# Kernel tuning notes

Hardware: AMD Instinct MI355X
Metric: run time of the kernel (lower is better)

The kernel has to match this reference:

```python
import jax, jax.numpy as jnp
import numpy as np

N, E, XD = 100000, 300000, 32
H, C = 4, 64          # heads, per-head out channels
D = H * C             # 256, node feature width
L = 3                 # num_message_passing
EPS = 1e-5
NEG_SLOPE = 0.2


def setup_inputs() -> dict:
    key = jax.random.key(0)
    ks = jax.random.split(key, 16)
    s = 0.05
    return {
        "x": jax.random.normal(ks[0], (N, XD), jnp.float32),
        "edge_index": jax.random.randint(ks[1], (2, E), 0, N, jnp.int32),
        "edge_type": jax.random.randint(ks[2], (E,), 0, 3, jnp.int32),
        "edge_feat": jax.random.uniform(ks[3], (E,), jnp.float32),
        # pre-encoder Linear(x_dim -> D)
        "W0": jax.random.normal(ks[4], (XD, D), jnp.float32) * s,
        "b0": jnp.zeros((D,), jnp.float32),
        # per-layer GATv2 params, stacked over L layers
        "Wl": jax.random.normal(ks[5], (L, D, D), jnp.float32) * s,
        "bl": jnp.zeros((L, D), jnp.float32),
        "Wr": jax.random.normal(ks[6], (L, D, D), jnp.float32) * s,
        "br": jnp.zeros((L, D), jnp.float32),
        "We": jax.random.normal(ks[7], (L, 4, D), jnp.float32) * s,  # lin_edge (no bias)
        "att": jax.random.normal(ks[8], (L, H, C), jnp.float32) * s,
        "bo": jnp.zeros((L, D), jnp.float32),
        # graph-mode LayerNorm (single module, reused every layer)
        "gamma": jnp.ones((D,), jnp.float32),
        "beta": jnp.zeros((D,), jnp.float32),
    }


def _graph_layernorm(h, gamma, beta):
    # PyG LayerNorm(mode='graph'): normalize over ALL nodes and features of the graph
    mu = jnp.mean(h)
    hc = h - mu
    var = jnp.mean(hc * hc)
    return hc * jax.lax.rsqrt(var + EPS) * gamma + beta


def _gatv2_layer(h, src, dst, eattr, Wl, bl, Wr, br, We, att, bo):
    xl = (h @ Wl + bl).reshape(N, H, C)
    xr = (h @ Wr + br).reshape(N, H, C)
    ea = (eattr @ We).reshape(E, H, C)
    e = jax.nn.leaky_relu(xl[src] + xr[dst] + ea, NEG_SLOPE)   # [E,H,C]
    alpha = jnp.einsum('ehc,hc->eh', e, att)                    # [E,H]
    amax = jax.ops.segment_max(alpha, dst, num_segments=N)     # [N,H]
    ex = jnp.exp(alpha - amax[dst])
    denom = jax.ops.segment_sum(ex, dst, num_segments=N)       # [N,H]
    a = ex / denom[dst]                                         # softmax per dst node
    msg = xl[src] * a[:, :, None]                               # [E,H,C]
    out = jax.ops.segment_sum(msg, dst, num_segments=N)        # [N,H,C]
    return out.reshape(N, D) + bo


def reference(x, edge_index, edge_type, edge_feat,
              W0, b0, Wl, bl, Wr, br, We, att, bo, gamma, beta):
    # edge feature construction: one-hot(type over 3) ++ scalar feature (== torch cat/where path)
    eattr = jnp.concatenate(
        [jax.nn.one_hot(edge_type, 3, dtype=x.dtype), edge_feat[:, None]], axis=-1)  # [E,4]
    src, dst = edge_index[0], edge_index[1]   # messages flow src -> dst
    h = jax.nn.relu(x @ W0 + b0)              # pre_enc (dropout = identity in eval)
    for i in range(L):
        g = _gatv2_layer(h, src, dst, eattr, Wl[i], bl[i], Wr[i], br[i], We[i], att[i], bo[i])
        h = _graph_layernorm(jax.nn.relu(g), gamma, beta)
    return h
```

## Files before the change

### kernel.cpp

```cpp
#include <hip/hip_runtime.h>
#include <hip/hip_bf16.h>

#define NN 100000
#define EE 300000
#define DD 256
#define HH 4
#define CC 64
#define LL 3
#define SCAN_CHUNK 1024

#define BM 64
#define BK 64
#define MPAD 100096

typedef __attribute__((ext_vector_type(8))) short bh8;
typedef __attribute__((ext_vector_type(4))) float f32x4;

__device__ inline float bf2f(unsigned short u) {
    union { float f; unsigned int i; } c; c.i = ((unsigned int)u) << 16; return c.f;
}
__device__ inline unsigned short f2bf(float x) {
    __hip_bfloat16 b = __float2bfloat16(x);
    return *reinterpret_cast<unsigned short*>(&b);
}


__global__ __launch_bounds__(256) void k_count(const int* __restrict__ dst, int* __restrict__ deg, int E_) {
    int e = blockIdx.x * 256 + threadIdx.x;
    if (e < E_) atomicAdd(&deg[dst[e]], 1);
}

__global__ __launch_bounds__(256) void k_scan1(const int* __restrict__ deg, int* __restrict__ bsum, int n) {
    int b = blockIdx.x;
    int base = b * SCAN_CHUNK;
    int t = threadIdx.x;
    int s = 0;
    for (int i = t; i < SCAN_CHUNK; i += 256) {
        int idx = base + i;
        if (idx < n) s += deg[idx];
    }
    __shared__ int sdata[256];
    sdata[t] = s;
    __syncthreads();
    for (int off = 128; off > 0; off >>= 1) {
        if (t < off) sdata[t] += sdata[t + off];
        __syncthreads();
    }
    if (t == 0) bsum[b] = sdata[0];
}

__global__ void k_scan2(const int* __restrict__ bsum, int* __restrict__ boff, int nb,
                        int* __restrict__ offsets, int n) {
    if (threadIdx.x == 0 && blockIdx.x == 0) {
        int run = 0;
        for (int i = 0; i < nb; i++) { boff[i] = run; run += bsum[i]; }
        offsets[n] = run;
    }
}

__global__ __launch_bounds__(256) void k_scan3(const int* __restrict__ deg, const int* __restrict__ boff,
                                               int* __restrict__ offsets, int n) {
    int b = blockIdx.x, t = threadIdx.x;
    int base = b * SCAN_CHUNK;
    int i0 = base + t * 4;
    int v[4]; int sum = 0;
    #pragma unroll
    for (int j = 0; j < 4; j++) {
        int idx = i0 + j;
        v[j] = (idx < n) ? deg[idx] : 0;
        sum += v[j];
    }
    __shared__ int sdata[256];
    sdata[t] = sum;
    __syncthreads();
    for (int off = 1; off < 256; off <<= 1) {
        int x = (t >= off) ? sdata[t - off] : 0;
        __syncthreads();
        sdata[t] += x;
        __syncthreads();
    }
    int excl = (t == 0) ? 0 : sdata[t - 1];
    int run = boff[b] + excl;
    #pragma unroll
    for (int j = 0; j < 4; j++) {
        int idx = i0 + j;
        if (idx < n) offsets[idx] = run;
        run += v[j];
    }
}

__global__ __launch_bounds__(256) void k_fill(const int* __restrict__ src, const int* __restrict__ dst,
                                              const int* __restrict__ ety, const float* __restrict__ efe,
                                              const int* __restrict__ offsets, int* __restrict__ cursor,
                                              int* __restrict__ csr_src, float* __restrict__ csr_feat, int E_) {
    int e = blockIdx.x * 256 + threadIdx.x;
    if (e < E_) {
        int d = dst[e];
        int pos = offsets[d] + atomicAdd(&cursor[d], 1);
        csr_src[pos] = src[e] | (ety[e] << 24);
        csr_feat[pos] = efe[e];
    }
}

__global__ __launch_bounds__(256) void k_cvtw(const float* __restrict__ Wl, const float* __restrict__ Wr,
                                              unsigned short* __restrict__ Wct) {
    int mat = blockIdx.z;
    int layer = mat >> 1, which = mat & 1;
    const float* src = (which ? Wr : Wl) + (size_t)layer * DD * DD;
    unsigned short* dst = Wct + (size_t)layer * 512 * DD + (size_t)which * DD * DD;
    int k0 = blockIdx.x * 64, n0 = blockIdx.y * 64;
    __shared__ float tile[64][65];
    int tx = threadIdx.x & 63, ty = threadIdx.x >> 6;
    #pragma unroll
    for (int i = 0; i < 16; i++) {
        int r = i * 4 + ty;
        tile[r][tx] = src[(size_t)(k0 + r) * DD + n0 + tx];
    }
    __syncthreads();
    #pragma unroll
    for (int i = 0; i < 16; i++) {
        int r = i * 4 + ty;
        dst[(size_t)(n0 + r) * DD + k0 + tx] = f2bf(tile[tx][r]);
    }
}

__global__ __launch_bounds__(256) void k_bias(const float* __restrict__ bl, const float* __restrict__ br,
                                              float* __restrict__ bc) {
    int i = blockIdx.x * 256 + threadIdx.x;
    if (i < LL * 512) {
        int l = i >> 9, j = i & 511;
        bc[i] = (j < 256) ? bl[l * DD + j] : br[l * DD + j - 256];
    }
}

__global__ __launch_bounds__(256) void k_preenc(const float* __restrict__ x, const float* __restrict__ W0,
                                                const float* __restrict__ b0, unsigned short* __restrict__ act) {
    __shared__ float xs[8][32];
    int t = threadIdx.x;
    int nb = blockIdx.x * 8;
    {
        int m = t >> 5, k = t & 31;
        xs[m][k] = x[(size_t)(nb + m) * 32 + k];
    }
    __syncthreads();
    float acc[8];
    float b = b0[t];
    #pragma unroll
    for (int m = 0; m < 8; m++) acc[m] = b;
    for (int k = 0; k < 32; k++) {
        float w = W0[k * DD + t];
        #pragma unroll
        for (int m = 0; m < 8; m++) acc[m] += xs[m][k] * w;
    }
    #pragma unroll
    for (int m = 0; m < 8; m++) {
        act[(size_t)(nb + m) * DD + t] = f2bf(fmaxf(acc[m], 0.f));
    }
}

__global__ __launch_bounds__(512) void k_gemm(const unsigned short* __restrict__ act,
                                              const unsigned short* __restrict__ Wct,
                                              const float* __restrict__ bc,
                                              unsigned short* __restrict__ xlr) {
    __shared__ short As[BM][68];
    __shared__ short Bs[512][68];
    short* stage = &Bs[0][0];
    int t = threadIdx.x;
    int lane = t & 63;
    int w = t >> 6;
    size_t rowBase = (size_t)blockIdx.x * BM;
    int rsel = lane & 15, kq = lane >> 4;

    f32x4 acc[4][4];
    #pragma unroll
    for (int i = 0; i < 4; i++)
        #pragma unroll
        for (int j = 0; j < 4; j++)
            acc[i][j] = (f32x4){0.f, 0.f, 0.f, 0.f};

    for (int ks = 0; ks < 4; ++ks) {
        __syncthreads();
        {
            int row = t >> 3, c8 = t & 7;
            *(bh8*)&As[row][c8 * 8] =
                *(const bh8*)(act + (rowBase + row) * DD + ks * BK + c8 * 8);
        }
        #pragma unroll
        for (int j = 0; j < 8; ++j) {
            int idx = t + j * 512;
            int row = idx >> 3, c8 = idx & 7;
            *(bh8*)&Bs[row][c8 * 8] =
                *(const bh8*)(Wct + (size_t)row * DD + ks * BK + c8 * 8);
        }
        __syncthreads();
        #pragma unroll
        for (int kk = 0; kk < BK; kk += 32) {
            bh8 af[4], bfr[4];
            int ksel = kk + kq * 8;
            #pragma unroll
            for (int mi = 0; mi < 4; mi++)
                af[mi] = *(const bh8*)&As[mi * 16 + rsel][ksel];
            #pragma unroll
            for (int ni = 0; ni < 4; ni++)
                bfr[ni] = *(const bh8*)&Bs[w * 64 + ni * 16 + rsel][ksel];
            #pragma unroll
            for (int mi = 0; mi < 4; mi++)
                #pragma unroll
                for (int ni = 0; ni < 4; ni++)
                    acc[mi][ni] = __builtin_amdgcn_mfma_f32_16x16x32_bf16(af[mi], bfr[ni], acc[mi][ni], 0, 0, 0);
        }
    }

    __syncthreads();
    #pragma unroll
    for (int ni = 0; ni < 4; ni++) {
        int col = w * 64 + ni * 16 + rsel;
        float bias = bc[col];
        #pragma unroll
        for (int mi = 0; mi < 4; mi++) {
            int r0 = mi * 16 + kq * 4;
            #pragma unroll
            for (int j = 0; j < 4; j++)
                stage[(r0 + j) * 544 + col] = (short)f2bf(acc[mi][ni][j] + bias);
        }
    }
    __syncthreads();
    #pragma unroll
    for (int j = 0; j < 8; ++j) {
        int idx = t + j * 512;
        int row = idx >> 6, c16 = idx & 63;
        size_t grow = rowBase + row;
        if (grow < NN)
            *(bh8*)(xlr + grow * 512 + c16 * 8) = *(const bh8*)&stage[row * 544 + c16 * 8];
    }
}

__global__ __launch_bounds__(256) void k_aggregate(const unsigned short* __restrict__ xlr,
                                                   const int* __restrict__ offsets,
                                                   const int* __restrict__ csr_src, const float* __restrict__ csr_feat,
                                                   const float* __restrict__ We, const float* __restrict__ att,
                                                   const float* __restrict__ bo,
                                                   unsigned short* __restrict__ act, float2* __restrict__ partial) {
    int lane = threadIdx.x & 63;
    int n = blockIdx.x * 4 + (threadIdx.x >> 6);
    int c0 = lane * 4;

    float4 attv = *(const float4*)(att + c0);
    float4 we3 = *(const float4*)(We + 3 * DD + c0);
    float4 w0v = *(const float4*)(We + 0 * DD + c0);
    float4 w1v = *(const float4*)(We + 1 * DD + c0);
    float4 w2v = *(const float4*)(We + 2 * DD + c0);

    uint2 xrr = *(const uint2*)(xlr + (size_t)n * 512 + 256 + c0);
    float xr0 = bf2f((unsigned short)(xrr.x & 0xffff));
    float xr1 = bf2f((unsigned short)(xrr.x >> 16));
    float xr2 = bf2f((unsigned short)(xrr.y & 0xffff));
    float xr3 = bf2f((unsigned short)(xrr.y >> 16));

    float b00 = xr0 + w0v.x, b01 = xr1 + w0v.y, b02 = xr2 + w0v.z, b03 = xr3 + w0v.w;
    float b10 = xr0 + w1v.x, b11 = xr1 + w1v.y, b12 = xr2 + w1v.z, b13 = xr3 + w1v.w;
    float b20 = xr0 + w2v.x, b21 = xr1 + w2v.y, b22 = xr2 + w2v.z, b23 = xr3 + w2v.w;

    int start = offsets[n], end = offsets[n + 1];
    float s = 0.f, a0 = 0.f, a1 = 0.f, a2 = 0.f, a3 = 0.f;
    int i = start;
    for (; i + 2 <= end; i += 2) {
        int pA = csr_src[i];     float fA = csr_feat[i];
        int pB = csr_src[i + 1]; float fB = csr_feat[i + 1];
        uint2 xvA = *(const uint2*)(xlr + (size_t)(pA & 0xFFFFF) * 512 + c0);
        uint2 xvB = *(const uint2*)(xlr + (size_t)(pB & 0xFFFFF) * 512 + c0);
        int tyA = pA >> 24, tyB = pB >> 24;
        float xA0 = bf2f((unsigned short)(xvA.x & 0xffff));
        float xA1 = bf2f((unsigned short)(xvA.x >> 16));
        float xA2 = bf2f((unsigned short)(xvA.y & 0xffff));
        float xA3 = bf2f((unsigned short)(xvA.y >> 16));
        float xB0 = bf2f((unsigned short)(xvB.x & 0xffff));
        float xB1 = bf2f((unsigned short)(xvB.x >> 16));
        float xB2 = bf2f((unsigned short)(xvB.y & 0xffff));
        float xB3 = bf2f((unsigned short)(xvB.y >> 16));
        float sA0 = (tyA == 0) ? b00 : (tyA == 1) ? b10 : b20;
        float sA1 = (tyA == 0) ? b01 : (tyA == 1) ? b11 : b21;
        float sA2 = (tyA == 0) ? b02 : (tyA == 1) ? b12 : b22;
        float sA3 = (tyA == 0) ? b03 : (tyA == 1) ? b13 : b23;
        float sB0 = (tyB == 0) ? b00 : (tyB == 1) ? b10 : b20;
        float sB1 = (tyB == 0) ? b01 : (tyB == 1) ? b11 : b21;
        float sB2 = (tyB == 0) ? b02 : (tyB == 1) ? b12 : b22;
        float sB3 = (tyB == 0) ? b03 : (tyB == 1) ? b13 : b23;
        float eA0 = xA0 + fmaf(fA, we3.x, sA0); eA0 = fmaxf(eA0, 0.2f * eA0);
        float eA1 = xA1 + fmaf(fA, we3.y, sA1); eA1 = fmaxf(eA1, 0.2f * eA1);
        float eA2 = xA2 + fmaf(fA, we3.z, sA2); eA2 = fmaxf(eA2, 0.2f * eA2);
        float eA3 = xA3 + fmaf(fA, we3.w, sA3); eA3 = fmaxf(eA3, 0.2f * eA3);
        float eB0 = xB0 + fmaf(fB, we3.x, sB0); eB0 = fmaxf(eB0, 0.2f * eB0);
        float eB1 = xB1 + fmaf(fB, we3.y, sB1); eB1 = fmaxf(eB1, 0.2f * eB1);
        float eB2 = xB2 + fmaf(fB, we3.z, sB2); eB2 = fmaxf(eB2, 0.2f * eB2);
        float eB3 = xB3 + fmaf(fB, we3.w, sB3); eB3 = fmaxf(eB3, 0.2f * eB3);
        float dA = attv.x * eA0 + attv.y * eA1 + attv.z * eA2 + attv.w * eA3;
        float dB = attv.x * eB0 + attv.y * eB1 + attv.z * eB2 + attv.w * eB3;
        dA += __shfl_xor(dA, 1, 64);  dB += __shfl_xor(dB, 1, 64);
        dA += __shfl_xor(dA, 2, 64);  dB += __shfl_xor(dB, 2, 64);
        dA += __shfl_xor(dA, 4, 64);  dB += __shfl_xor(dB, 4, 64);
        dA += __shfl_xor(dA, 8, 64);  dB += __shfl_xor(dB, 8, 64);
        float pa = __expf(fminf(fmaxf(dA, -60.f), 60.f));
        float pb = __expf(fminf(fmaxf(dB, -60.f), 60.f));
        s += pa + pb;
        a0 = fmaf(pa, xA0, fmaf(pb, xB0, a0));
        a1 = fmaf(pa, xA1, fmaf(pb, xB1, a1));
        a2 = fmaf(pa, xA2, fmaf(pb, xB2, a2));
        a3 = fmaf(pa, xA3, fmaf(pb, xB3, a3));
    }
    if (i < end) {
        int pA = csr_src[i]; float fA = csr_feat[i];
        uint2 xvA = *(const uint2*)(xlr + (size_t)(pA & 0xFFFFF) * 512 + c0);
        int tyA = pA >> 24;
        float xA0 = bf2f((unsigned short)(xvA.x & 0xffff));
        float xA1 = bf2f((unsigned short)(xvA.x >> 16));
        float xA2 = bf2f((unsigned short)(xvA.y & 0xffff));
        float xA3 = bf2f((unsigned short)(xvA.y >> 16));
        float sA0 = (tyA == 0) ? b00 : (tyA == 1) ? b10 : b20;
        float sA1 = (tyA == 0) ? b01 : (tyA == 1) ? b11 : b21;
        float sA2 = (tyA == 0) ? b02 : (tyA == 1) ? b12 : b22;
        float sA3 = (tyA == 0) ? b03 : (tyA == 1) ? b13 : b23;
        float eA0 = xA0 + fmaf(fA, we3.x, sA0); eA0 = fmaxf(eA0, 0.2f * eA0);
        float eA1 = xA1 + fmaf(fA, we3.y, sA1); eA1 = fmaxf(eA1, 0.2f * eA1);
        float eA2 = xA2 + fmaf(fA, we3.z, sA2); eA2 = fmaxf(eA2, 0.2f * eA2);
        float eA3 = xA3 + fmaf(fA, we3.w, sA3); eA3 = fmaxf(eA3, 0.2f * eA3);
        float dA = attv.x * eA0 + attv.y * eA1 + attv.z * eA2 + attv.w * eA3;
        dA += __shfl_xor(dA, 1, 64);
        dA += __shfl_xor(dA, 2, 64);
        dA += __shfl_xor(dA, 4, 64);
        dA += __shfl_xor(dA, 8, 64);
        float pa = __expf(fminf(fmaxf(dA, -60.f), 60.f));
        s += pa;
        a0 = fmaf(pa, xA0, a0);
        a1 = fmaf(pa, xA1, a1);
        a2 = fmaf(pa, xA2, a2);
        a3 = fmaf(pa, xA3, a3);
    }
    float inv = (end > start) ? __builtin_amdgcn_rcpf(s) : 0.f;
    float4 bov = *(const float4*)(bo + c0);
    float o0 = fmaxf(fmaf(a0, inv, bov.x), 0.f);
    float o1 = fmaxf(fmaf(a1, inv, bov.y), 0.f);
    float o2 = fmaxf(fmaf(a2, inv, bov.z), 0.f);
    float o3 = fmaxf(fmaf(a3, inv, bov.w), 0.f);
    uint2 pk;
    pk.x = (unsigned int)f2bf(o0) | ((unsigned int)f2bf(o1) << 16);
    pk.y = (unsigned int)f2bf(o2) | ((unsigned int)f2bf(o3) << 16);
    *(uint2*)(act + (size_t)n * DD + c0) = pk;

    float v1 = o0 + o1 + o2 + o3;
    float v2 = o0 * o0 + o1 * o1 + o2 * o2 + o3 * o3;
    #pragma unroll
    for (int off = 32; off > 0; off >>= 1) {
        v1 += __shfl_xor(v1, off, 64);
        v2 += __shfl_xor(v2, off, 64);
    }
    if (lane == 0) partial[n] = make_float2(v1, v2);
}

__global__ __launch_bounds__(256) void k_lnreduce(const float2* __restrict__ partial,
                                                  double2* __restrict__ partial2) {
    int b = blockIdx.x, t = threadIdx.x;
    double s1 = 0.0, s2 = 0.0;
    for (int i = b * 256 + t; i < NN; i += 64 * 256) {
        float2 p = partial[i];
        s1 += p.x; s2 += p.y;
    }
    __shared__ double d1[256], d2[256];
    d1[t] = s1; d2[t] = s2;
    __syncthreads();
    for (int off = 128; off > 0; off >>= 1) {
        if (t < off) { d1[t] += d1[t + off]; d2[t] += d2[t + off]; }
        __syncthreads();
    }
    if (t == 0) partial2[b] = (double2){d1[0], d2[0]};
}

__global__ __launch_bounds__(256) void k_stats(const double2* __restrict__ partial2,
                                               const float* __restrict__ gamma, const float* __restrict__ beta,
                                               float* __restrict__ sc, float* __restrict__ vsh) {
    __shared__ double d1[64], d2[64];
    int t = threadIdx.x;
    if (t < 64) { double2 p = partial2[t]; d1[t] = p.x; d2[t] = p.y; }
    __syncthreads();
    for (int off = 32; off > 0; off >>= 1) {
        if (t < off) { d1[t] += d1[t + off]; d2[t] += d2[t + off]; }
        __syncthreads();
    }
    const double M = (double)NN * DD;
    double mu = d1[0] / M;
    double var = d2[0] / M - mu * mu;
    float rs = rsqrtf((float)(var + 1e-5));
    float scv = rs * gamma[t];
    sc[t] = scv;
    vsh[t] = beta[t] - (float)mu * scv;
}

__global__ __launch_bounds__(256) void k_foldw(const unsigned short* __restrict__ Wct,
                                               const float* __restrict__ bcL,
                                               const float* __restrict__ sc, const float* __restrict__ vsh,
                                               unsigned short* __restrict__ Wct2, float* __restrict__ bc2) {
    int row = (blockIdx.x << 2) + (threadIdx.x >> 6);
    int lane = threadIdx.x & 63;
    int k0 = lane * 4;
    uint2 raw = *(const uint2*)(Wct + (size_t)row * DD + k0);
    float w0 = bf2f((unsigned short)(raw.x & 0xffff));
    float w1 = bf2f((unsigned short)(raw.x >> 16));
    float w2 = bf2f((unsigned short)(raw.y & 0xffff));
    float w3 = bf2f((unsigned short)(raw.y >> 16));
    float4 scv = *(const float4*)(sc + k0);
    float4 vv  = *(const float4*)(vsh + k0);
    uint2 pk;
    pk.x = (unsigned int)f2bf(w0 * scv.x) | ((unsigned int)f2bf(w1 * scv.y) << 16);
    pk.y = (unsigned int)f2bf(w2 * scv.z) | ((unsigned int)f2bf(w3 * scv.w) << 16);
    *(uint2*)(Wct2 + (size_t)row * DD + k0) = pk;
    float d = w0 * vv.x + w1 * vv.y + w2 * vv.z + w3 * vv.w;
    #pragma unroll
    for (int off = 32; off > 0; off >>= 1) d += __shfl_xor(d, off, 64);
    if (lane == 0) bc2[row] = bcL[row] + d;
}

__global__ __launch_bounds__(256) void k_final(const unsigned short* __restrict__ act,
                                               const float* __restrict__ sc, const float* __restrict__ vsh,
                                               float* __restrict__ h) {
    size_t i = ((size_t)blockIdx.x * 256 + threadIdx.x) * 4;
    uint2 raw = *(const uint2*)(act + i);
    int ch = (int)(i & (DD - 1));
    float4 scv = *(const float4*)(sc + ch);
    float4 vv  = *(const float4*)(vsh + ch);
    float4 o;
    o.x = fmaf(bf2f((unsigned short)(raw.x & 0xffff)), scv.x, vv.x);
    o.y = fmaf(bf2f((unsigned short)(raw.x >> 16)),    scv.y, vv.y);
    o.z = fmaf(bf2f((unsigned short)(raw.y & 0xffff)), scv.z, vv.z);
    o.w = fmaf(bf2f((unsigned short)(raw.y >> 16)),    scv.w, vv.w);
    *reinterpret_cast<float4*>(h + i) = o;
}


extern "C" void kernel_launch(void* const* d_in, const int* in_sizes, int n_in,
                              void* d_out, int out_size, void* d_ws, size_t ws_size,
                              hipStream_t stream) {
    const float* x    = (const float*)d_in[0];
    const int*   ei   = (const int*)d_in[1];
    const int*   ety  = (const int*)d_in[2];
    const float* efe  = (const float*)d_in[3];
    const float* W0   = (const float*)d_in[4];
    const float* b0   = (const float*)d_in[5];
    const float* Wl   = (const float*)d_in[6];
    const float* bl   = (const float*)d_in[7];
    const float* Wr   = (const float*)d_in[8];
    const float* br   = (const float*)d_in[9];
    const float* We   = (const float*)d_in[10];
    const float* att  = (const float*)d_in[11];
    const float* bo   = (const float*)d_in[12];
    const float* gamma= (const float*)d_in[13];
    const float* beta = (const float*)d_in[14];
    float* h = (float*)d_out;

    char* base = (char*)d_ws;
    size_t off = 0;
    auto carve = [&](size_t bytes) -> void* {
        void* p = base + off;
        off += (bytes + 255) & ~(size_t)255;
        return p;
    };
    unsigned short* act  = (unsigned short*)carve((size_t)MPAD * DD * 2);
    unsigned short* xlr  = (unsigned short*)carve((size_t)NN * 512 * 2);
    unsigned short* Wct  = (unsigned short*)carve((size_t)LL * 512 * DD * 2);
    unsigned short* Wct2 = (unsigned short*)carve((size_t)512 * DD * 2);
    float* bc            = (float*)carve((size_t)LL * 512 * 4);
    float* bc2           = (float*)carve((size_t)512 * 4);
    float* sc            = (float*)carve((size_t)DD * 4);
    float* vsh           = (float*)carve((size_t)DD * 4);
    int*   deg      = (int*)carve((size_t)NN * 4);
    int*   offsets  = (int*)carve((size_t)(NN + 1) * 4);
    int*   bsum     = (int*)carve(1024);
    int*   boff     = (int*)carve(1024);
    int*   csr_src  = (int*)carve((size_t)EE * 4);
    float* csr_feat = (float*)carve((size_t)EE * 4);
    float2* partial = (float2*)carve((size_t)NN * 8);
    double2* partial2 = (double2*)carve((size_t)64 * 16);

    const int NB = (NN + SCAN_CHUNK - 1) / SCAN_CHUNK;

    hipMemsetAsync(deg, 0, (size_t)NN * 4, stream);
    k_count<<<(EE + 255) / 256, 256, 0, stream>>>(ei + EE, deg, EE);
    k_scan1<<<NB, 256, 0, stream>>>(deg, bsum, NN);
    k_scan2<<<1, 64, 0, stream>>>(bsum, boff, NB, offsets, NN);
    k_scan3<<<NB, 256, 0, stream>>>(deg, boff, offsets, NN);
    hipMemsetAsync(deg, 0, (size_t)NN * 4, stream);
    k_fill<<<(EE + 255) / 256, 256, 0, stream>>>(ei, ei + EE, ety, efe, offsets, deg,
                                                 csr_src, csr_feat, EE);

    k_cvtw<<<dim3(4, 4, 6), 256, 0, stream>>>(Wl, Wr, Wct);
    k_bias<<<6, 256, 0, stream>>>(bl, br, bc);

    k_preenc<<<NN / 8, 256, 0, stream>>>(x, W0, b0, act);

    for (int l = 0; l < LL; l++) {
        const unsigned short* Wg = (l == 0) ? Wct : Wct2;
        const float* bg = (l == 0) ? bc : bc2;
        k_gemm<<<MPAD / BM, 512, 0, stream>>>(act, Wg, bg, xlr);
        k_aggregate<<<NN / 4, 256, 0, stream>>>(xlr, offsets, csr_src, csr_feat,
                                                We + (size_t)l * 4 * DD, att + (size_t)l * HH * CC,
                                                bo + (size_t)l * DD, act, partial);
        k_lnreduce<<<64, 256, 0, stream>>>(partial, partial2);
        k_stats<<<1, 256, 0, stream>>>(partial2, gamma, beta, sc, vsh);
        if (l < LL - 1)
            k_foldw<<<128, 256, 0, stream>>>(Wct + (size_t)(l + 1) * 512 * DD, bc + (size_t)(l + 1) * 512,
                                             sc, vsh, Wct2, bc2);
    }
    k_final<<<(NN * DD / 4) / 256, 256, 0, stream>>>(act, sc, vsh, h);
}
```

Measured before the change: 524.1 us.

## Retile GEMM to 128x128 tiles with register-prefetched B fragments from global

The fused Wl/Wr GEMM changes from 64-row blocks that each staged the full 512-column weight in LDS to a 2D grid of 128x128 output tiles with 256 threads. Activation halves are loaded into LDS while B fragments are read directly from global memory into registers, one k-step ahead. This cuts LDS footprint and per-block weight staging so more blocks can be resident. In exchange, A is re-read once per column tile and B fragment loads rely on cache.

Result: slower. 542.0 us (+3.4%).

```diff
diff --git a/kernel.cpp b/kernel.cpp
--- a/kernel.cpp
+++ b/kernel.cpp
@@ -9,8 +9,6 @@
 #define LL 3
 #define SCAN_CHUNK 1024
 
-#define BM 64
-#define BK 64
 #define MPAD 100096
 
 typedef __attribute__((ext_vector_type(8))) short bh8;
@@ -158,18 +156,20 @@
     }
 }
 
-__global__ __launch_bounds__(512) void k_gemm(const unsigned short* __restrict__ act,
-                                              const unsigned short* __restrict__ Wct,
-                                              const float* __restrict__ bc,
-                                              unsigned short* __restrict__ xlr) {
-    __shared__ short As[BM][68];
-    __shared__ short Bs[512][68];
-    short* stage = &Bs[0][0];
+__global__ __launch_bounds__(256, 3) void k_gemm(const unsigned short* __restrict__ act,
+                                                 const unsigned short* __restrict__ Wct,
+                                                 const float* __restrict__ bc,
+                                                 unsigned short* __restrict__ xlr) {
+    __shared__ short As[128][136];
     int t = threadIdx.x;
     int lane = t & 63;
     int w = t >> 6;
-    size_t rowBase = (size_t)blockIdx.x * BM;
+    int wm = w >> 1, wn = w & 1;
+    size_t rowBase = (size_t)blockIdx.x * 128;
+    int n0 = blockIdx.y * 128;
     int rsel = lane & 15, kq = lane >> 4;
+
+    const unsigned short* Bw = Wct + (size_t)(n0 + wn * 64) * DD;
 
     f32x4 acc[4][4];
     #pragma unroll
@@ -178,60 +178,75 @@
         for (int j = 0; j < 4; j++)
             acc[i][j] = (f32x4){0.f, 0.f, 0.f, 0.f};
 
-    for (int ks = 0; ks < 4; ++ks) {
-        __syncthreads();
-        {
-            int row = t >> 3, c8 = t & 7;
-            *(bh8*)&As[row][c8 * 8] =
-                *(const bh8*)(act + (rowBase + row) * DD + ks * BK + c8 * 8);
+    #pragma unroll
+    for (int j = 0; j < 8; j++) {
+        int idx = t + j * 256;
+        int row = idx >> 4, c = idx & 15;
+        *(bh8*)&As[row][c * 8] = *(const bh8*)(act + (rowBase + row) * DD + c * 8);
+    }
+
+    bh8 bcur[4], bnxt[4];
+    #pragma unroll
+    for (int ni = 0; ni < 4; ni++)
+        bcur[ni] = *(const bh8*)(Bw + (size_t)(ni * 16 + rsel) * DD + kq * 8);
+
+    __syncthreads();
+
+    #pragma unroll
+    for (int s = 0; s < 8; ++s) {
+        if (s == 4) {
+            __syncthreads();
+            #pragma unroll
+            for (int j = 0; j < 8; j++) {
+                int idx = t + j * 256;
+                int row = idx >> 4, c = idx & 15;
+                *(bh8*)&As[row][c * 8] = *(const bh8*)(act + (rowBase + row) * DD + 128 + c * 8);
+            }
+            __syncthreads();
         }
-        #pragma unroll
-        for (int j = 0; j < 8; ++j) {
-            int idx = t + j * 512;
-            int row = idx >> 3, c8 = idx & 7;
-            *(bh8*)&Bs[row][c8 * 8] =
-                *(const bh8*)(Wct + (size_t)row * DD + ks * BK + c8 * 8);
-        }
-        __syncthreads();
-        #pragma unroll
-        for (int kk = 0; kk < BK; kk += 32) {
-            bh8 af[4], bfr[4];
-            int ksel = kk + kq * 8;
-            #pragma unroll
-            for (int mi = 0; mi < 4; mi++)
-                af[mi] = *(const bh8*)&As[mi * 16 + rsel][ksel];
+        if (s < 7) {
+            int s2 = s + 1;
+            int kb2 = (s2 >> 2) * 128 + (s2 & 3) * 32 + kq * 8;
             #pragma unroll
             for (int ni = 0; ni < 4; ni++)
-                bfr[ni] = *(const bh8*)&Bs[w * 64 + ni * 16 + rsel][ksel];
+                bnxt[ni] = *(const bh8*)(Bw + (size_t)(ni * 16 + rsel) * DD + kb2);
+        }
+        int ksel = (s & 3) * 32 + kq * 8;
+        bh8 af[4];
+        #pragma unroll
+        for (int mi = 0; mi < 4; mi++)
+            af[mi] = *(const bh8*)&As[wm * 64 + mi * 16 + rsel][ksel];
+        #pragma unroll
+        for (int mi = 0; mi < 4; mi++)
             #pragma unroll
-            for (int mi = 0; mi < 4; mi++)
-                #pragma unroll
-                for (int ni = 0; ni < 4; ni++)
-                    acc[mi][ni] = __builtin_amdgcn_mfma_f32_16x16x32_bf16(af[mi], bfr[ni], acc[mi][ni], 0, 0, 0);
-        }
-    }
-
-    __syncthreads();
+            for (int ni = 0; ni < 4; ni++)
+                acc[mi][ni] = __builtin_amdgcn_mfma_f32_16x16x32_bf16(af[mi], bcur[ni], acc[mi][ni], 0, 0, 0);
+        #pragma unroll
+        for (int ni = 0; ni < 4; ni++) bcur[ni] = bnxt[ni];
+    }
+
+    __syncthreads();
+    short* stage = &As[0][0];
     #pragma unroll
     for (int ni = 0; ni < 4; ni++) {
-        int col = w * 64 + ni * 16 + rsel;
-        float bias = bc[col];
+        int col = wn * 64 + ni * 16 + rsel;
+        float bias = bc[n0 + col];
         #pragma unroll
         for (int mi = 0; mi < 4; mi++) {
-            int r0 = mi * 16 + kq * 4;
+            int r0 = wm * 64 + mi * 16 + kq * 4;
             #pragma unroll
             for (int j = 0; j < 4; j++)
-                stage[(r0 + j) * 544 + col] = (short)f2bf(acc[mi][ni][j] + bias);
+                stage[(r0 + j) * 136 + col] = (short)f2bf(acc[mi][ni][j] + bias);
         }
     }
     __syncthreads();
     #pragma unroll
-    for (int j = 0; j < 8; ++j) {
-        int idx = t + j * 512;
-        int row = idx >> 6, c16 = idx & 63;
+    for (int j = 0; j < 8; j++) {
+        int idx = t + j * 256;
+        int row = idx >> 4, c = idx & 15;
         size_t grow = rowBase + row;
         if (grow < NN)
-            *(bh8*)(xlr + grow * 512 + c16 * 8) = *(const bh8*)&stage[row * 544 + c16 * 8];
+            *(bh8*)(xlr + grow * 512 + n0 + c * 8) = *(const bh8*)&stage[row * 136 + c * 8];
     }
 }
 
@@ -499,7 +514,7 @@
     for (int l = 0; l < LL; l++) {
         const unsigned short* Wg = (l == 0) ? Wct : Wct2;
         const float* bg = (l == 0) ? bc : bc2;
-        k_gemm<<<MPAD / BM, 512, 0, stream>>>(act, Wg, bg, xlr);
+        k_gemm<<<dim3(MPAD / 128, 4), 256, 0, stream>>>(act, Wg, bg, xlr);
         k_aggregate<<<NN / 4, 256, 0, stream>>>(xlr, offsets, csr_src, csr_feat,
                                                 We + (size_t)l * 4 * DD, att + (size_t)l * HH * CC,
                                                 bo + (size_t)l * DD, act, partial);
```

## Double-buffer GEMM K-loop with direct global-to-LDS loads and XOR swizzle

Applied to the files above, without the earlier changes.

Restructures the node GEMM's K loop from four 64-wide steps into eight 32-wide steps with ping-pong LDS buffers. The next tile is loaded while MFMAs run on the current one, using global_load_lds so data goes straight into shared memory without passing through registers. An XOR swizzle on the 16-byte column groups replaces row padding to avoid LDS bank conflicts, and launch bounds now request 4 blocks per SM. This cuts the load-then-compute stalls and one barrier per step, at the cost of more, smaller iterations and a tighter fit in LDS.

Result: no change. 528.3 us (+0.8%).

```diff
diff --git a/kernel.cpp b/kernel.cpp
--- a/kernel.cpp
+++ b/kernel.cpp
@@ -9,8 +9,6 @@
 #define LL 3
 #define SCAN_CHUNK 1024
 
-#define BM 64
-#define BK 64
 #define MPAD 100096
 
 typedef __attribute__((ext_vector_type(8))) short bh8;
@@ -22,6 +20,12 @@
 __device__ inline unsigned short f2bf(float x) {
     __hip_bfloat16 b = __float2bfloat16(x);
     return *reinterpret_cast<unsigned short*>(&b);
+}
+
+typedef const __attribute__((address_space(1))) unsigned int* gas1;
+typedef __attribute__((address_space(3))) unsigned int* las3;
+__device__ __forceinline__ void gld16(const unsigned short* g, const short* lds_wave_base) {
+    __builtin_amdgcn_global_load_lds((gas1)(uintptr_t)g, (las3)(uintptr_t)lds_wave_base, 16, 0, 0);
 }
 
 
@@ -158,17 +162,19 @@
     }
 }
 
-__global__ __launch_bounds__(512) void k_gemm(const unsigned short* __restrict__ act,
-                                              const unsigned short* __restrict__ Wct,
-                                              const float* __restrict__ bc,
-                                              unsigned short* __restrict__ xlr) {
-    __shared__ short As[BM][68];
-    __shared__ short Bs[512][68];
-    short* stage = &Bs[0][0];
+__global__ __launch_bounds__(512, 4) void k_gemm(const unsigned short* __restrict__ act,
+                                                 const unsigned short* __restrict__ Wct,
+                                                 const float* __restrict__ bc,
+                                                 unsigned short* __restrict__ xlr) {
+    __shared__ short lds[36864];
+    short* B0 = lds;
+    short* B1 = lds + 16384;
+    short* A0 = lds + 32768;
+    short* A1 = lds + 34816;
     int t = threadIdx.x;
     int lane = t & 63;
     int w = t >> 6;
-    size_t rowBase = (size_t)blockIdx.x * BM;
+    size_t rowBase = (size_t)blockIdx.x * 64;
     int rsel = lane & 15, kq = lane >> 4;
 
     f32x4 acc[4][4];
@@ -178,40 +184,52 @@
         for (int j = 0; j < 4; j++)
             acc[i][j] = (f32x4){0.f, 0.f, 0.f, 0.f};
 
-    for (int ks = 0; ks < 4; ++ks) {
-        __syncthreads();
-        {
-            int row = t >> 3, c8 = t & 7;
-            *(bh8*)&As[row][c8 * 8] =
-                *(const bh8*)(act + (rowBase + row) * DD + ks * BK + c8 * 8);
+    auto stage = [&](int ks, short* Ab, short* Bb) {
+        #pragma unroll
+        for (int j = 0; j < 4; ++j) {
+            int slot = t + j * 512;
+            int row = slot >> 2, cs = slot & 3;
+            int cg = cs ^ (row & 3);
+            gld16(Wct + (size_t)row * DD + ks * 32 + cg * 8,
+                  Bb + (size_t)(j * 512 + w * 64) * 8);
         }
-        #pragma unroll
-        for (int j = 0; j < 8; ++j) {
-            int idx = t + j * 512;
-            int row = idx >> 3, c8 = idx & 7;
-            *(bh8*)&Bs[row][c8 * 8] =
-                *(const bh8*)(Wct + (size_t)row * DD + ks * BK + c8 * 8);
+        if (t < 256) {
+            int row = t >> 2, cs = t & 3;
+            int cg = cs ^ (row & 3);
+            gld16(act + (rowBase + row) * DD + ks * 32 + cg * 8,
+                  Ab + (size_t)(w * 64) * 8);
         }
-        __syncthreads();
-        #pragma unroll
-        for (int kk = 0; kk < BK; kk += 32) {
-            bh8 af[4], bfr[4];
-            int ksel = kk + kq * 8;
-            #pragma unroll
-            for (int mi = 0; mi < 4; mi++)
-                af[mi] = *(const bh8*)&As[mi * 16 + rsel][ksel];
+    };
+
+    stage(0, A0, B0);
+    __syncthreads();
+
+    #pragma unroll
+    for (int ks = 0; ks < 8; ++ks) {
+        short* Ab = (ks & 1) ? A1 : A0;
+        short* Bb = (ks & 1) ? B1 : B0;
+        if (ks < 7) stage(ks + 1, (ks & 1) ? A0 : A1, (ks & 1) ? B0 : B1);
+
+        bh8 af[4], bfr[4];
+        #pragma unroll
+        for (int mi = 0; mi < 4; mi++) {
+            int row = mi * 16 + rsel;
+            af[mi] = *(const bh8*)&Ab[row * 32 + (kq ^ (row & 3)) * 8];
+        }
+        #pragma unroll
+        for (int ni = 0; ni < 4; ni++) {
+            int row = w * 64 + ni * 16 + rsel;
+            bfr[ni] = *(const bh8*)&Bb[row * 32 + (kq ^ (row & 3)) * 8];
+        }
+        #pragma unroll
+        for (int mi = 0; mi < 4; mi++)
             #pragma unroll
             for (int ni = 0; ni < 4; ni++)
-                bfr[ni] = *(const bh8*)&Bs[w * 64 + ni * 16 + rsel][ksel];
-            #pragma unroll
-            for (int mi = 0; mi < 4; mi++)
-                #pragma unroll
-                for (int ni = 0; ni < 4; ni++)
-                    acc[mi][ni] = __builtin_amdgcn_mfma_f32_16x16x32_bf16(af[mi], bfr[ni], acc[mi][ni], 0, 0, 0);
-        }
-    }
-
-    __syncthreads();
+                acc[mi][ni] = __builtin_amdgcn_mfma_f32_16x16x32_bf16(af[mi], bfr[ni], acc[mi][ni], 0, 0, 0);
+
+        __syncthreads();
+    }
+
     #pragma unroll
     for (int ni = 0; ni < 4; ni++) {
         int col = w * 64 + ni * 16 + rsel;
@@ -221,7 +239,7 @@
             int r0 = mi * 16 + kq * 4;
             #pragma unroll
             for (int j = 0; j < 4; j++)
-                stage[(r0 + j) * 544 + col] = (short)f2bf(acc[mi][ni][j] + bias);
+                lds[(r0 + j) * 544 + col] = (short)f2bf(acc[mi][ni][j] + bias);
         }
     }
     __syncthreads();
@@ -231,7 +249,7 @@
         int row = idx >> 6, c16 = idx & 63;
         size_t grow = rowBase + row;
         if (grow < NN)
-            *(bh8*)(xlr + grow * 512 + c16 * 8) = *(const bh8*)&stage[row * 544 + c16 * 8];
+            *(bh8*)(xlr + grow * 512 + c16 * 8) = *(const bh8*)&lds[row * 544 + c16 * 8];
     }
 }
 
@@ -499,7 +517,7 @@
     for (int l = 0; l < LL; l++) {
         const unsigned short* Wg = (l == 0) ? Wct : Wct2;
         const float* bg = (l == 0) ? bc : bc2;
-        k_gemm<<<MPAD / BM, 512, 0, stream>>>(act, Wg, bg, xlr);
+        k_gemm<<<MPAD / 64, 512, 0, stream>>>(act, Wg, bg, xlr);
         k_aggregate<<<NN / 4, 256, 0, stream>>>(xlr, offsets, csr_src, csr_feat,
                                                 We + (size_t)l * 4 * DD, att + (size_t)l * HH * CC,
                                                 bo + (size_t)l * DD, act, partial);
```

## Register-prefetch next K-slice in GEMM and shrink LDS tiles to BK=32

Applied to the files above, without the earlier changes.

The node-feature GEMM kernel now uses K-slices of 32 instead of 64 and loads the next slice from global memory into registers while the MFMAs of the current slice run, then stores it to LDS after a barrier. The LDS tile footprint drops from about 78 KB to about 66 KB with a single shared buffer, so more blocks may fit per CU. The goal is to hide global-load latency behind compute. The cost is twice as many barriers per tile, extra register pressure from the prefetch registers, and reuse of the same LDS region for the output staging.

Result: slower. 867.9 us (+65.6%).

```diff
diff --git a/kernel.cpp b/kernel.cpp
--- a/kernel.cpp
+++ b/kernel.cpp
@@ -9,8 +9,6 @@
 #define LL 3
 #define SCAN_CHUNK 1024
 
-#define BM 64
-#define BK 64
 #define MPAD 100096
 
 typedef __attribute__((ext_vector_type(8))) short bh8;
@@ -162,14 +160,19 @@
                                               const unsigned short* __restrict__ Wct,
                                               const float* __restrict__ bc,
                                               unsigned short* __restrict__ xlr) {
-    __shared__ short As[BM][68];
-    __shared__ short Bs[512][68];
-    short* stage = &Bs[0][0];
+    __shared__ short lds[33024];
+    short* Bb = lds;
+    short* Ab = lds + 512 * 36;
     int t = threadIdx.x;
     int lane = t & 63;
     int w = t >> 6;
-    size_t rowBase = (size_t)blockIdx.x * BM;
+    size_t rowBase = (size_t)blockIdx.x * 64;
     int rsel = lane & 15, kq = lane >> 4;
+
+    int r0 = t >> 2, cs = t & 3;
+    const unsigned short* gB = Wct + (size_t)r0 * DD + cs * 8;
+    const unsigned short* gA = act + (rowBase + r0) * DD + cs * 8;
+    int d0 = r0 * 36 + cs * 8;
 
     f32x4 acc[4][4];
     #pragma unroll
@@ -178,50 +181,65 @@
         for (int j = 0; j < 4; j++)
             acc[i][j] = (f32x4){0.f, 0.f, 0.f, 0.f};
 
-    for (int ks = 0; ks < 4; ++ks) {
-        __syncthreads();
-        {
-            int row = t >> 3, c8 = t & 7;
-            *(bh8*)&As[row][c8 * 8] =
-                *(const bh8*)(act + (rowBase + row) * DD + ks * BK + c8 * 8);
+    {
+        bh8 rB0 = *(const bh8*)(gB);
+        bh8 rB1 = *(const bh8*)(gB + 32768);
+        bh8 rB2 = *(const bh8*)(gB + 65536);
+        bh8 rB3 = *(const bh8*)(gB + 98304);
+        bh8 rA;
+        if (t < 256) rA = *(const bh8*)(gA);
+        *(bh8*)&Bb[d0]          = rB0;
+        *(bh8*)&Bb[d0 + 4608]   = rB1;
+        *(bh8*)&Bb[d0 + 9216]   = rB2;
+        *(bh8*)&Bb[d0 + 13824]  = rB3;
+        if (t < 256) *(bh8*)&Ab[d0] = rA;
+    }
+    __syncthreads();
+
+    #pragma unroll
+    for (int ks = 0; ks < 8; ++ks) {
+        bh8 nB0, nB1, nB2, nB3, nA;
+        if (ks < 7) {
+            int ko = (ks + 1) * 32;
+            nB0 = *(const bh8*)(gB + ko);
+            nB1 = *(const bh8*)(gB + 32768 + ko);
+            nB2 = *(const bh8*)(gB + 65536 + ko);
+            nB3 = *(const bh8*)(gB + 98304 + ko);
+            if (t < 256) nA = *(const bh8*)(gA + ko);
         }
+        bh8 af[4], bfr[4];
         #pragma unroll
-        for (int j = 0; j < 8; ++j) {
-            int idx = t + j * 512;
-            int row = idx >> 3, c8 = idx & 7;
-            *(bh8*)&Bs[row][c8 * 8] =
-                *(const bh8*)(Wct + (size_t)row * DD + ks * BK + c8 * 8);
-        }
-        __syncthreads();
+        for (int mi = 0; mi < 4; mi++)
+            af[mi] = *(const bh8*)&Ab[(mi * 16 + rsel) * 36 + kq * 8];
         #pragma unroll
-        for (int kk = 0; kk < BK; kk += 32) {
-            bh8 af[4], bfr[4];
-            int ksel = kk + kq * 8;
-            #pragma unroll
-            for (int mi = 0; mi < 4; mi++)
-                af[mi] = *(const bh8*)&As[mi * 16 + rsel][ksel];
+        for (int ni = 0; ni < 4; ni++)
+            bfr[ni] = *(const bh8*)&Bb[(w * 64 + ni * 16 + rsel) * 36 + kq * 8];
+        #pragma unroll
+        for (int mi = 0; mi < 4; mi++)
             #pragma unroll
             for (int ni = 0; ni < 4; ni++)
-                bfr[ni] = *(const bh8*)&Bs[w * 64 + ni * 16 + rsel][ksel];
-            #pragma unroll
-            for (int mi = 0; mi < 4; mi++)
-                #pragma unroll
-                for (int ni = 0; ni < 4; ni++)
-                    acc[mi][ni] = __builtin_amdgcn_mfma_f32_16x16x32_bf16(af[mi], bfr[ni], acc[mi][ni], 0, 0, 0);
+                acc[mi][ni] = __builtin_amdgcn_mfma_f32_16x16x32_bf16(af[mi], bfr[ni], acc[mi][ni], 0, 0, 0);
+        __syncthreads();
+        if (ks < 7) {
+            *(bh8*)&Bb[d0]          = nB0;
+            *(bh8*)&Bb[d0 + 4608]   = nB1;
+            *(bh8*)&Bb[d0 + 9216]   = nB2;
+            *(bh8*)&Bb[d0 + 13824]  = nB3;
+            if (t < 256) *(bh8*)&Ab[d0] = nA;
+            __syncthreads();
         }
     }
 
-    __syncthreads();
     #pragma unroll
     for (int ni = 0; ni < 4; ni++) {
         int col = w * 64 + ni * 16 + rsel;
         float bias = bc[col];
         #pragma unroll
         for (int mi = 0; mi < 4; mi++) {
-            int r0 = mi * 16 + kq * 4;
+            int re = mi * 16 + kq * 4;
             #pragma unroll
             for (int j = 0; j < 4; j++)
-                stage[(r0 + j) * 544 + col] = (short)f2bf(acc[mi][ni][j] + bias);
+                lds[(re + j) * 516 + col] = (short)f2bf(acc[mi][ni][j] + bias);
         }
     }
     __syncthreads();
@@ -231,7 +249,7 @@
         int row = idx >> 6, c16 = idx & 63;
         size_t grow = rowBase + row;
         if (grow < NN)
-            *(bh8*)(xlr + grow * 512 + c16 * 8) = *(const bh8*)&stage[row * 544 + c16 * 8];
+            *(bh8*)(xlr + grow * 512 + c16 * 8) = *(const bh8*)&lds[row * 516 + c16 * 8];
     }
 }
 
@@ -499,7 +517,7 @@
     for (int l = 0; l < LL; l++) {
         const unsigned short* Wg = (l == 0) ? Wct : Wct2;
         const float* bg = (l == 0) ? bc : bc2;
-        k_gemm<<<MPAD / BM, 512, 0, stream>>>(act, Wg, bg, xlr);
+        k_gemm<<<MPAD / 64, 512, 0, stream>>>(act, Wg, bg, xlr);
         k_aggregate<<<NN / 4, 256, 0, stream>>>(xlr, offsets, csr_src, csr_feat,
                                                 We + (size_t)l * 4 * DD, att + (size_t)l * HH * CC,
                                                 bo + (size_t)l * DD, act, partial);
```
